# Optimization experiments

Measured on AMD Instinct MI355X. Metric: run time of the kernel, lower is better.

The kernel has to match this reference:

```python
import jax, jax.numpy as jnp
import numpy as np


def setup_inputs() -> dict:
    key = jax.random.key(0)
    kq, kk, kv = jax.random.split(key, 3)
    B, N, D = 8, 4096, 128
    Q = jax.random.normal(kq, (B, N, D), dtype=jnp.float32)
    K = jax.random.normal(kk, (B, N, D), dtype=jnp.float32)
    V = jax.random.normal(kv, (B, N, D), dtype=jnp.float32)
    return {"Q": Q, "K": K, "V": V}


def reference(Q, K, V):
    # attention = Q @ K^T  -> [B, N, N]  (scale=None, mask=None path)
    attention = jnp.einsum('bnd,bmd->bnm', Q, K)
    attention = jax.nn.softmax(attention, axis=-1)
    # context = attention @ V -> [B, N, D]
    context = jnp.einsum('bnm,bmd->bnd', attention, V)
    return context
```

## Files before the change

### kernel.cpp

```cpp
#include <hip/hip_runtime.h>

#define NB 8
#define SEQ 4096
#define DIM 128
#define BQ 128
#define KVB 64
#define NTILES (SEQ / KVB)
#define ROUNDS (NTILES / 2)
#define IMG_BYTES 32768
#define WS_NEED ((size_t)NB * NTILES * IMG_BYTES)
#define L2E 1.44269504088896f

typedef _Float16 f16x8 __attribute__((ext_vector_type(8)));
typedef __bf16 bf16x8 __attribute__((ext_vector_type(8)));
typedef float f32x4 __attribute__((ext_vector_type(4)));
typedef float f32x16 __attribute__((ext_vector_type(16)));

struct U4 { unsigned x, y, z, w; };

static __device__ __forceinline__ unsigned cvtpk_bf16(float a, float b) {
  unsigned d;
  asm("v_cvt_pk_bf16_f32 %0, %1, %2" : "=v"(d) : "v"(a), "v"(b));
  return d;
}

#define EXP2(x) __builtin_amdgcn_exp2f(x)

__global__ void prep_kv(const float* __restrict__ K, const float* __restrict__ V,
                        unsigned char* __restrict__ ws) {
  const int t = blockIdx.x;
  const int b = blockIdx.y;
  unsigned char* img = ws + ((size_t)b * NTILES + t) * IMG_BYTES;
  int4* kimg = (int4*)img;
  int4* vimg = (int4*)(img + 16384);
  const float* Kb = K + ((size_t)b * SEQ + t * KVB) * DIM;
  const float* Vb = V + ((size_t)b * SEQ + t * KVB) * DIM;
  const int tid = threadIdx.x;

#pragma unroll
  for (int p = 0; p < 4; ++p) {
    const int un = tid + 256 * p;
    const int kv = un >> 4;
    const int u = (un & 15) ^ (kv & 7);
    const int s = u >> 1, hh = u & 1;
    const float* src = Kb + (size_t)kv * DIM + 16 * s + 8 * hh;
    f16x8 hv;
#pragma unroll
    for (int j = 0; j < 8; ++j) hv[j] = (_Float16)src[j];
    kimg[un] = __builtin_bit_cast(int4, hv);
  }

#pragma unroll
  for (int p = 0; p < 4; ++p) {
    const int un = tid + 256 * p;
    const int d = un >> 3;
    const int u = (un & 7) ^ (d & 7);
    const int s2 = u >> 1, hh = u & 1;
    bf16x8 hv;
#pragma unroll
    for (int e = 0; e < 8; ++e) {
      const int kv = 16 * s2 + 4 * hh + (e & 3) + 8 * (e >> 2);
      hv[e] = (__bf16)Vb[(size_t)kv * DIM + d];
    }
    vimg[un] = __builtin_bit_cast(int4, hv);
  }
}

__global__ __launch_bounds__(512, 2)
void attn_fwd9(const float* __restrict__ Q, const unsigned char* __restrict__ ws,
               float* __restrict__ O) {
  __shared__ __align__(16) unsigned char smem[131072];

  const int tid = threadIdx.x;
  const int grp = tid >> 8;
  const int w4 = (tid >> 6) & 3;
  const int l = tid & 63;
  const int l31 = l & 31;
  const int h = l >> 5;

  const int bid = blockIdx.x;
  const int b = bid & 7;
  const int qt = bid >> 3;
  const size_t base = (size_t)b * SEQ * DIM;
  const int qrow = qt * BQ + w4 * 32 + l31;

  f16x8 qf[8];
  {
    const float* qp = Q + base + (size_t)qrow * DIM + 8 * h;
#pragma unroll
    for (int s = 0; s < 8; ++s) {
      f32x4 a = *(const f32x4*)(qp + 16 * s);
      f32x4 c = *(const f32x4*)(qp + 16 * s + 4);
      f16x8 hv;
#pragma unroll
      for (int j = 0; j < 4; ++j) {
        hv[j] = (_Float16)(a[j] * L2E);
        hv[j + 4] = (_Float16)(c[j] * L2E);
      }
      qf[s] = hv;
    }
  }

  f32x16 o[4];
#pragma unroll
  for (int j = 0; j < 4; ++j) {
#pragma unroll
    for (int r = 0; r < 16; ++r) o[j][r] = 0.f;
  }
  float ls = 0.f;

  unsigned char* mybuf = smem + grp * 65536;
  const unsigned char* wsb = ws + (size_t)b * NTILES * IMG_BYTES;

  auto STAGE = [&](int t, int bufsel) {
    const unsigned char* src = wsb + (size_t)t * IMG_BYTES + w4 * 8192 + l * 16;
    unsigned char* dst = mybuf + bufsel * 32768 + w4 * 8192;
#pragma unroll
    for (int i = 0; i < 8; ++i) {
      __builtin_amdgcn_global_load_lds(
          (const __attribute__((address_space(1))) unsigned int*)(src + i * 1024),
          (__attribute__((address_space(3))) unsigned int*)(dst + i * 1024),
          16, 0, 0);
    }
  };

  const int kb2 = (l31 * 256 + ((l & 7) * 16)) ^ (h * 16);
  const int vb2 = (16384 + l31 * 128 + ((l & 7) * 16)) ^ (h * 16);

  STAGE(grp, 0);
  __syncthreads();

  for (int i = 0; i < ROUNDS; ++i) {
    const int cur = i & 1;
    if (i + 1 < ROUNDS) STAGE(2 * (i + 1) + grp, cur ^ 1);
    const unsigned char* bufp = mybuf + cur * 32768;

    f32x16 s0, s1;
#pragma unroll
    for (int r = 0; r < 16; ++r) { s0[r] = 0.f; s1[r] = 0.f; }
    __builtin_amdgcn_s_setprio(1);
#pragma unroll
    for (int s = 0; s < 8; ++s) {
      const unsigned char* ka = bufp + (kb2 ^ (32 * s));
      f16x8 k0 = *(const f16x8*)(ka);
      f16x8 k1 = *(const f16x8*)(ka + 8192);
      s0 = __builtin_amdgcn_mfma_f32_32x32x16_f16(k0, qf[s], s0, 0, 0, 0);
      s1 = __builtin_amdgcn_mfma_f32_32x32x16_f16(k1, qf[s], s1, 0, 0, 0);
    }
    __builtin_amdgcn_s_setprio(0);

    float a0 = 0.f, a1 = 0.f, a2 = 0.f, a3 = 0.f;
#pragma unroll
    for (int r = 0; r < 16; r += 4) {
      s0[r + 0] = EXP2(s0[r + 0]);
      s0[r + 1] = EXP2(s0[r + 1]);
      s0[r + 2] = EXP2(s0[r + 2]);
      s0[r + 3] = EXP2(s0[r + 3]);
      a0 += s0[r + 0]; a1 += s0[r + 1]; a2 += s0[r + 2]; a3 += s0[r + 3];
    }
#pragma unroll
    for (int r = 0; r < 16; r += 4) {
      s1[r + 0] = EXP2(s1[r + 0]);
      s1[r + 1] = EXP2(s1[r + 1]);
      s1[r + 2] = EXP2(s1[r + 2]);
      s1[r + 3] = EXP2(s1[r + 3]);
      a0 += s1[r + 0]; a1 += s1[r + 1]; a2 += s1[r + 2]; a3 += s1[r + 3];
    }
    ls += (a0 + a1) + (a2 + a3);

    bf16x8 pb[2][2];
#pragma unroll
    for (int u = 0; u < 2; ++u) {
      U4 t0 = {cvtpk_bf16(s0[8 * u + 0], s0[8 * u + 1]),
               cvtpk_bf16(s0[8 * u + 2], s0[8 * u + 3]),
               cvtpk_bf16(s0[8 * u + 4], s0[8 * u + 5]),
               cvtpk_bf16(s0[8 * u + 6], s0[8 * u + 7])};
      U4 t1 = {cvtpk_bf16(s1[8 * u + 0], s1[8 * u + 1]),
               cvtpk_bf16(s1[8 * u + 2], s1[8 * u + 3]),
               cvtpk_bf16(s1[8 * u + 4], s1[8 * u + 5]),
               cvtpk_bf16(s1[8 * u + 6], s1[8 * u + 7])};
      pb[0][u] = __builtin_bit_cast(bf16x8, t0);
      pb[1][u] = __builtin_bit_cast(bf16x8, t1);
    }

    __builtin_amdgcn_s_setprio(1);
#pragma unroll
    for (int s2 = 0; s2 < 4; ++s2) {
      const unsigned char* va = bufp + (vb2 ^ (32 * s2));
      const bf16x8 pbb = pb[s2 >> 1][s2 & 1];
#pragma unroll
      for (int j = 0; j < 4; ++j) {
        bf16x8 vf = *(const bf16x8*)(va + j * 4096);
        o[j] = __builtin_amdgcn_mfma_f32_32x32x16_bf16(vf, pbb, o[j], 0, 0, 0);
      }
    }
    __builtin_amdgcn_s_setprio(0);
    __syncthreads();
  }

  ls += __shfl_xor(ls, 32);

  if (grp == 1) {
    int4* park = (int4*)(smem + w4 * 16384);
#pragma unroll
    for (int j = 0; j < 4; ++j) {
#pragma unroll
      for (int rq = 0; rq < 4; ++rq) {
        f32x4 part = {o[j][4 * rq + 0], o[j][4 * rq + 1], o[j][4 * rq + 2],
                      o[j][4 * rq + 3]};
        park[l * 16 + ((4 * j + rq) ^ (l & 7))] = __builtin_bit_cast(int4, part);
      }
    }
    if (h == 0) *(float*)(smem + 65536 + w4 * 128 + l31 * 4) = ls;
  }
  __syncthreads();

  if (grp == 0) {
    const float lsB = *(const float*)(smem + 65536 + w4 * 128 + l31 * 4);
    const float inv = 1.0f / (ls + lsB);
    const int4* park = (const int4*)(smem + w4 * 16384);
    float* Ob = O + base + (size_t)qrow * DIM;
#pragma unroll
    for (int j = 0; j < 4; ++j) {
#pragma unroll
      for (int rq = 0; rq < 4; ++rq) {
        const f32x4 ob =
            __builtin_bit_cast(f32x4, park[l * 16 + ((4 * j + rq) ^ (l & 7))]);
        f32x4 res;
#pragma unroll
        for (int r = 0; r < 4; ++r)
          res[r] = (o[j][4 * rq + r] + ob[r]) * inv;
        *(f32x4*)(Ob + 32 * j + 8 * rq + 4 * h) = res;
      }
    }
  }
}

extern "C" void kernel_launch(void* const* d_in, const int* in_sizes, int n_in,
                              void* d_out, int out_size, void* d_ws,
                              size_t ws_size, hipStream_t stream) {
  const float* Q = (const float*)d_in[0];
  const float* K = (const float*)d_in[1];
  const float* V = (const float*)d_in[2];
  float* Out = (float*)d_out;
  if (ws_size < WS_NEED) return;
  prep_kv<<<dim3(NTILES, NB), dim3(256), 0, stream>>>(K, V, (unsigned char*)d_ws);
  attn_fwd9<<<dim3(SEQ / BQ * NB), dim3(512), 0, stream>>>(
      Q, (const unsigned char*)d_ws, Out);
}
```

Measured before the change: 96.12 us.

## Widen K/V LDS swizzle to 16 and interleave softmax with PV MFMAs per sub-tile

Changes the K and V workspace image layout to use a 16-way XOR swizzle, with V laid out as 256-byte rows covering two 64-dim halves, to cut LDS bank conflicts on the fragment reads. It also splits the QK MFMA loop into two sequential chains and processes the first 32-key sub-tile's exp/convert/PV MFMAs before the second sub-tile's exp. The intent is to overlap transcendental work with matrix-core work and shorten dependency stalls. The risks are a longer serial MFMA chain in the QK step and higher register pressure from the precomputed V offsets.

New measurement: 94.47 us. No clear change (-1.7%).

```diff
diff --git a/kernel.cpp b/kernel.cpp
--- a/kernel.cpp
+++ b/kernel.cpp
@@ -41,7 +41,7 @@
   for (int p = 0; p < 4; ++p) {
     const int un = tid + 256 * p;
     const int kv = un >> 4;
-    const int u = (un & 15) ^ (kv & 7);
+    const int u = (un & 15) ^ (kv & 15);
     const int s = u >> 1, hh = u & 1;
     const float* src = Kb + (size_t)kv * DIM + 16 * s + 8 * hh;
     f16x8 hv;
@@ -53,9 +53,11 @@
 #pragma unroll
   for (int p = 0; p < 4; ++p) {
     const int un = tid + 256 * p;
-    const int d = un >> 3;
-    const int u = (un & 7) ^ (d & 7);
-    const int s2 = u >> 1, hh = u & 1;
+    const int rr = un >> 4;
+    const int c = (un & 15) ^ (rr & 15);
+    const int dhi = c >> 3, slot = c & 7;
+    const int s2 = slot >> 1, hh = slot & 1;
+    const int d = 64 * dhi + rr;
     bf16x8 hv;
 #pragma unroll
     for (int e = 0; e < 8; ++e) {
@@ -67,8 +69,8 @@
 }
 
 __global__ __launch_bounds__(512, 2)
-void attn_fwd9(const float* __restrict__ Q, const unsigned char* __restrict__ ws,
-               float* __restrict__ O) {
+void attn_fwd10(const float* __restrict__ Q, const unsigned char* __restrict__ ws,
+                float* __restrict__ O) {
   __shared__ __align__(16) unsigned char smem[131072];
 
   const int tid = threadIdx.x;
@@ -124,8 +126,13 @@
     }
   };
 
-  const int kb2 = (l31 * 256 + ((l & 7) * 16)) ^ (h * 16);
-  const int vb2 = (16384 + l31 * 128 + ((l & 7) * 16)) ^ (h * 16);
+  const int kb2 = (l31 * 256 + ((l31 & 15) * 16)) ^ (h * 16);
+  int vb[4];
+#pragma unroll
+  for (int j = 0; j < 4; ++j) {
+    const int rr = 32 * (j & 1) + l31;
+    vb[j] = 16384 + rr * 256 + ((((j >> 1) * 8 + h) ^ (rr & 15)) * 16);
+  }
 
   STAGE(grp, 0);
   __syncthreads();
@@ -141,10 +148,12 @@
     __builtin_amdgcn_s_setprio(1);
 #pragma unroll
     for (int s = 0; s < 8; ++s) {
-      const unsigned char* ka = bufp + (kb2 ^ (32 * s));
-      f16x8 k0 = *(const f16x8*)(ka);
-      f16x8 k1 = *(const f16x8*)(ka + 8192);
+      f16x8 k0 = *(const f16x8*)(bufp + (kb2 ^ (32 * s)));
       s0 = __builtin_amdgcn_mfma_f32_32x32x16_f16(k0, qf[s], s0, 0, 0, 0);
+    }
+#pragma unroll
+    for (int s = 0; s < 8; ++s) {
+      f16x8 k1 = *(const f16x8*)(bufp + (kb2 ^ (32 * s)) + 8192);
       s1 = __builtin_amdgcn_mfma_f32_32x32x16_f16(k1, qf[s], s1, 0, 0, 0);
     }
     __builtin_amdgcn_s_setprio(0);
@@ -158,6 +167,27 @@
       s0[r + 3] = EXP2(s0[r + 3]);
       a0 += s0[r + 0]; a1 += s0[r + 1]; a2 += s0[r + 2]; a3 += s0[r + 3];
     }
+    bf16x8 pb0[2];
+#pragma unroll
+    for (int u = 0; u < 2; ++u) {
+      U4 t0 = {cvtpk_bf16(s0[8 * u + 0], s0[8 * u + 1]),
+               cvtpk_bf16(s0[8 * u + 2], s0[8 * u + 3]),
+               cvtpk_bf16(s0[8 * u + 4], s0[8 * u + 5]),
+               cvtpk_bf16(s0[8 * u + 6], s0[8 * u + 7])};
+      pb0[u] = __builtin_bit_cast(bf16x8, t0);
+    }
+
+    __builtin_amdgcn_s_setprio(1);
+#pragma unroll
+    for (int s2 = 0; s2 < 2; ++s2) {
+#pragma unroll
+      for (int j = 0; j < 4; ++j) {
+        bf16x8 vf = *(const bf16x8*)(bufp + (vb[j] ^ (32 * s2)));
+        o[j] = __builtin_amdgcn_mfma_f32_32x32x16_bf16(vf, pb0[s2], o[j], 0, 0, 0);
+      }
+    }
+    __builtin_amdgcn_s_setprio(0);
+
 #pragma unroll
     for (int r = 0; r < 16; r += 4) {
       s1[r + 0] = EXP2(s1[r + 0]);
@@ -167,31 +197,23 @@
       a0 += s1[r + 0]; a1 += s1[r + 1]; a2 += s1[r + 2]; a3 += s1[r + 3];
     }
     ls += (a0 + a1) + (a2 + a3);
-
-    bf16x8 pb[2][2];
+    bf16x8 pb1[2];
 #pragma unroll
     for (int u = 0; u < 2; ++u) {
-      U4 t0 = {cvtpk_bf16(s0[8 * u + 0], s0[8 * u + 1]),
-               cvtpk_bf16(s0[8 * u + 2], s0[8 * u + 3]),
-               cvtpk_bf16(s0[8 * u + 4], s0[8 * u + 5]),
-               cvtpk_bf16(s0[8 * u + 6], s0[8 * u + 7])};
       U4 t1 = {cvtpk_bf16(s1[8 * u + 0], s1[8 * u + 1]),
                cvtpk_bf16(s1[8 * u + 2], s1[8 * u + 3]),
                cvtpk_bf16(s1[8 * u + 4], s1[8 * u + 5]),
                cvtpk_bf16(s1[8 * u + 6], s1[8 * u + 7])};
-      pb[0][u] = __builtin_bit_cast(bf16x8, t0);
-      pb[1][u] = __builtin_bit_cast(bf16x8, t1);
+      pb1[u] = __builtin_bit_cast(bf16x8, t1);
     }
 
     __builtin_amdgcn_s_setprio(1);
 #pragma unroll
-    for (int s2 = 0; s2 < 4; ++s2) {
-      const unsigned char* va = bufp + (vb2 ^ (32 * s2));
-      const bf16x8 pbb = pb[s2 >> 1][s2 & 1];
+    for (int s2 = 2; s2 < 4; ++s2) {
 #pragma unroll
       for (int j = 0; j < 4; ++j) {
-        bf16x8 vf = *(const bf16x8*)(va + j * 4096);
-        o[j] = __builtin_amdgcn_mfma_f32_32x32x16_bf16(vf, pbb, o[j], 0, 0, 0);
+        bf16x8 vf = *(const bf16x8*)(bufp + (vb[j] ^ (32 * s2)));
+        o[j] = __builtin_amdgcn_mfma_f32_32x32x16_bf16(vf, pb1[s2 - 2], o[j], 0, 0, 0);
       }
     }
     __builtin_amdgcn_s_setprio(0);
@@ -245,6 +267,6 @@
   float* Out = (float*)d_out;
   if (ws_size < WS_NEED) return;
   prep_kv<<<dim3(NTILES, NB), dim3(256), 0, stream>>>(K, V, (unsigned char*)d_ws);
-  attn_fwd9<<<dim3(SEQ / BQ * NB), dim3(512), 0, stream>>>(
+  attn_fwd10<<<dim3(SEQ / BQ * NB), dim3(512), 0, stream>>>(
       Q, (const unsigned char*)d_ws, Out);
 }
```

## Split KV loop across four wave groups with 32-row tiles and staged reduction

Applied to the files above, without the earlier changes.

Each block now has 1024 threads in four wave groups. Each group processes interleaved 32-row KV tiles instead of two groups on 64-row tiles, and the prep kernel's K/V image layout and swizzle are reworked to match. Per-wave accumulators are combined through a serialized four-stage LDS reduction before normalization and the store. The goal is more waves in flight per query tile to hide latency. In exchange there are more barriers, a longer epilogue reduction, and fewer blocks resident per CU (launch_bounds drops the min-2-blocks hint while LDS use stays at 128KB).

Measured after the change: 117.1 us. 21.9% more time.

```diff
diff --git a/kernel.cpp b/kernel.cpp
--- a/kernel.cpp
+++ b/kernel.cpp
@@ -4,10 +4,10 @@
 #define SEQ 4096
 #define DIM 128
 #define BQ 128
-#define KVB 64
+#define KVB 32
 #define NTILES (SEQ / KVB)
-#define ROUNDS (NTILES / 2)
-#define IMG_BYTES 32768
+#define ROUNDS (NTILES / 4)
+#define IMG_BYTES 16384
 #define WS_NEED ((size_t)NB * NTILES * IMG_BYTES)
 #define L2E 1.44269504088896f
 
@@ -32,17 +32,17 @@
   const int b = blockIdx.y;
   unsigned char* img = ws + ((size_t)b * NTILES + t) * IMG_BYTES;
   int4* kimg = (int4*)img;
-  int4* vimg = (int4*)(img + 16384);
+  int4* vimg = (int4*)(img + 8192);
   const float* Kb = K + ((size_t)b * SEQ + t * KVB) * DIM;
   const float* Vb = V + ((size_t)b * SEQ + t * KVB) * DIM;
   const int tid = threadIdx.x;
 
 #pragma unroll
-  for (int p = 0; p < 4; ++p) {
+  for (int p = 0; p < 2; ++p) {
     const int un = tid + 256 * p;
     const int kv = un >> 4;
-    const int u = (un & 15) ^ (kv & 7);
-    const int s = u >> 1, hh = u & 1;
+    const int c = (un & 15) ^ (kv & 15);
+    const int s = c >> 1, hh = c & 1;
     const float* src = Kb + (size_t)kv * DIM + 16 * s + 8 * hh;
     f16x8 hv;
 #pragma unroll
@@ -51,11 +51,12 @@
   }
 
 #pragma unroll
-  for (int p = 0; p < 4; ++p) {
+  for (int p = 0; p < 2; ++p) {
     const int un = tid + 256 * p;
-    const int d = un >> 3;
-    const int u = (un & 7) ^ (d & 7);
-    const int s2 = u >> 1, hh = u & 1;
+    const int rr = un >> 4;
+    const int c = (un & 15) ^ (rr & 15);
+    const int dhi = c >> 2, s2 = (c >> 1) & 1, hh = c & 1;
+    const int d = 32 * dhi + rr;
     bf16x8 hv;
 #pragma unroll
     for (int e = 0; e < 8; ++e) {
@@ -66,14 +67,15 @@
   }
 }
 
-__global__ __launch_bounds__(512, 2)
-void attn_fwd9(const float* __restrict__ Q, const unsigned char* __restrict__ ws,
-               float* __restrict__ O) {
+__global__ __launch_bounds__(1024)
+void attn_fwd11(const float* __restrict__ Q, const unsigned char* __restrict__ ws,
+                float* __restrict__ O) {
   __shared__ __align__(16) unsigned char smem[131072];
 
   const int tid = threadIdx.x;
-  const int grp = tid >> 8;
-  const int w4 = (tid >> 6) & 3;
+  const int w = tid >> 6;
+  const int g = w >> 2;
+  const int wg = w & 3;
   const int l = tid & 63;
   const int l31 = l & 31;
   const int h = l >> 5;
@@ -82,7 +84,7 @@
   const int b = bid & 7;
   const int qt = bid >> 3;
   const size_t base = (size_t)b * SEQ * DIM;
-  const int qrow = qt * BQ + w4 * 32 + l31;
+  const int qrow = qt * BQ + wg * 32 + l31;
 
   f16x8 qf[8];
   {
@@ -109,89 +111,71 @@
   }
   float ls = 0.f;
 
-  unsigned char* mybuf = smem + grp * 65536;
+  unsigned char* mybuf = smem + g * 32768;
   const unsigned char* wsb = ws + (size_t)b * NTILES * IMG_BYTES;
 
   auto STAGE = [&](int t, int bufsel) {
-    const unsigned char* src = wsb + (size_t)t * IMG_BYTES + w4 * 8192 + l * 16;
-    unsigned char* dst = mybuf + bufsel * 32768 + w4 * 8192;
-#pragma unroll
-    for (int i = 0; i < 8; ++i) {
+    const unsigned char* src = wsb + (size_t)t * IMG_BYTES + wg * 4096 + l * 16;
+    unsigned char* dst = mybuf + bufsel * 16384 + wg * 4096;
+#pragma unroll
+    for (int i2 = 0; i2 < 4; ++i2) {
       __builtin_amdgcn_global_load_lds(
-          (const __attribute__((address_space(1))) unsigned int*)(src + i * 1024),
-          (__attribute__((address_space(3))) unsigned int*)(dst + i * 1024),
+          (const __attribute__((address_space(1))) unsigned int*)(src + i2 * 1024),
+          (__attribute__((address_space(3))) unsigned int*)(dst + i2 * 1024),
           16, 0, 0);
     }
   };
 
-  const int kb2 = (l31 * 256 + ((l & 7) * 16)) ^ (h * 16);
-  const int vb2 = (16384 + l31 * 128 + ((l & 7) * 16)) ^ (h * 16);
-
-  STAGE(grp, 0);
+  const int lbase = l31 * 256 + ((((l31 & 15)) << 4) ^ (h << 4));
+
+  STAGE(g, 0);
   __syncthreads();
 
   for (int i = 0; i < ROUNDS; ++i) {
     const int cur = i & 1;
-    if (i + 1 < ROUNDS) STAGE(2 * (i + 1) + grp, cur ^ 1);
-    const unsigned char* bufp = mybuf + cur * 32768;
-
-    f32x16 s0, s1;
-#pragma unroll
-    for (int r = 0; r < 16; ++r) { s0[r] = 0.f; s1[r] = 0.f; }
+    if (i + 1 < ROUNDS) STAGE(4 * (i + 1) + g, cur ^ 1);
+    const unsigned char* bufp = mybuf + cur * 16384;
+
+    f32x16 s;
+#pragma unroll
+    for (int r = 0; r < 16; ++r) s[r] = 0.f;
     __builtin_amdgcn_s_setprio(1);
 #pragma unroll
-    for (int s = 0; s < 8; ++s) {
-      const unsigned char* ka = bufp + (kb2 ^ (32 * s));
-      f16x8 k0 = *(const f16x8*)(ka);
-      f16x8 k1 = *(const f16x8*)(ka + 8192);
-      s0 = __builtin_amdgcn_mfma_f32_32x32x16_f16(k0, qf[s], s0, 0, 0, 0);
-      s1 = __builtin_amdgcn_mfma_f32_32x32x16_f16(k1, qf[s], s1, 0, 0, 0);
+    for (int s8 = 0; s8 < 8; ++s8) {
+      f16x8 kf = *(const f16x8*)(bufp + (lbase ^ (s8 << 5)));
+      s = __builtin_amdgcn_mfma_f32_32x32x16_f16(kf, qf[s8], s, 0, 0, 0);
     }
     __builtin_amdgcn_s_setprio(0);
 
     float a0 = 0.f, a1 = 0.f, a2 = 0.f, a3 = 0.f;
 #pragma unroll
     for (int r = 0; r < 16; r += 4) {
-      s0[r + 0] = EXP2(s0[r + 0]);
-      s0[r + 1] = EXP2(s0[r + 1]);
-      s0[r + 2] = EXP2(s0[r + 2]);
-      s0[r + 3] = EXP2(s0[r + 3]);
-      a0 += s0[r + 0]; a1 += s0[r + 1]; a2 += s0[r + 2]; a3 += s0[r + 3];
-    }
-#pragma unroll
-    for (int r = 0; r < 16; r += 4) {
-      s1[r + 0] = EXP2(s1[r + 0]);
-      s1[r + 1] = EXP2(s1[r + 1]);
-      s1[r + 2] = EXP2(s1[r + 2]);
-      s1[r + 3] = EXP2(s1[r + 3]);
-      a0 += s1[r + 0]; a1 += s1[r + 1]; a2 += s1[r + 2]; a3 += s1[r + 3];
+      s[r + 0] = EXP2(s[r + 0]);
+      s[r + 1] = EXP2(s[r + 1]);
+      s[r + 2] = EXP2(s[r + 2]);
+      s[r + 3] = EXP2(s[r + 3]);
+      a0 += s[r + 0]; a1 += s[r + 1]; a2 += s[r + 2]; a3 += s[r + 3];
     }
     ls += (a0 + a1) + (a2 + a3);
 
-    bf16x8 pb[2][2];
+    bf16x8 pb[2];
 #pragma unroll
     for (int u = 0; u < 2; ++u) {
-      U4 t0 = {cvtpk_bf16(s0[8 * u + 0], s0[8 * u + 1]),
-               cvtpk_bf16(s0[8 * u + 2], s0[8 * u + 3]),
-               cvtpk_bf16(s0[8 * u + 4], s0[8 * u + 5]),
-               cvtpk_bf16(s0[8 * u + 6], s0[8 * u + 7])};
-      U4 t1 = {cvtpk_bf16(s1[8 * u + 0], s1[8 * u + 1]),
-               cvtpk_bf16(s1[8 * u + 2], s1[8 * u + 3]),
-               cvtpk_bf16(s1[8 * u + 4], s1[8 * u + 5]),
-               cvtpk_bf16(s1[8 * u + 6], s1[8 * u + 7])};
-      pb[0][u] = __builtin_bit_cast(bf16x8, t0);
-      pb[1][u] = __builtin_bit_cast(bf16x8, t1);
+      U4 t0 = {cvtpk_bf16(s[8 * u + 0], s[8 * u + 1]),
+               cvtpk_bf16(s[8 * u + 2], s[8 * u + 3]),
+               cvtpk_bf16(s[8 * u + 4], s[8 * u + 5]),
+               cvtpk_bf16(s[8 * u + 6], s[8 * u + 7])};
+      pb[u] = __builtin_bit_cast(bf16x8, t0);
     }
 
     __builtin_amdgcn_s_setprio(1);
 #pragma unroll
-    for (int s2 = 0; s2 < 4; ++s2) {
-      const unsigned char* va = bufp + (vb2 ^ (32 * s2));
-      const bf16x8 pbb = pb[s2 >> 1][s2 & 1];
+    for (int s2 = 0; s2 < 2; ++s2) {
 #pragma unroll
       for (int j = 0; j < 4; ++j) {
-        bf16x8 vf = *(const bf16x8*)(va + j * 4096);
-        o[j] = __builtin_amdgcn_mfma_f32_32x32x16_bf16(vf, pbb, o[j], 0, 0, 0);
+        bf16x8 vf = *(const bf16x8*)(bufp + 8192 +
+                                     (lbase ^ (j << 6) ^ (s2 << 5)));
+        o[j] = __builtin_amdgcn_mfma_f32_32x32x16_bf16(vf, pb[s2], o[j], 0, 0, 0);
       }
     }
     __builtin_amdgcn_s_setprio(0);
@@ -200,39 +184,58 @@
 
   ls += __shfl_xor(ls, 32);
 
-  if (grp == 1) {
-    int4* park = (int4*)(smem + w4 * 16384);
-#pragma unroll
-    for (int j = 0; j < 4; ++j) {
-#pragma unroll
-      for (int rq = 0; rq < 4; ++rq) {
-        f32x4 part = {o[j][4 * rq + 0], o[j][4 * rq + 1], o[j][4 * rq + 2],
-                      o[j][4 * rq + 3]};
-        park[l * 16 + ((4 * j + rq) ^ (l & 7))] = __builtin_bit_cast(int4, part);
+  int4* park = (int4*)(smem + wg * 16384);
+  float* lsp = (float*)(smem + 65536);
+  const int lsi = wg * 32 + l31;
+
+  __syncthreads();
+#pragma unroll 1
+  for (int stage = 0; stage < 4; ++stage) {
+    if (g == stage) {
+      if (stage == 0) {
+#pragma unroll
+        for (int j = 0; j < 4; ++j) {
+#pragma unroll
+          for (int rq = 0; rq < 4; ++rq) {
+            f32x4 part = {o[j][4 * rq + 0], o[j][4 * rq + 1],
+                          o[j][4 * rq + 2], o[j][4 * rq + 3]};
+            park[l * 16 + ((4 * j + rq) ^ (l & 7))] =
+                __builtin_bit_cast(int4, part);
+          }
+        }
+        if (h == 0) lsp[lsi] = ls;
+      } else if (stage < 3) {
+#pragma unroll
+        for (int j = 0; j < 4; ++j) {
+#pragma unroll
+          for (int rq = 0; rq < 4; ++rq) {
+            const int idx = l * 16 + ((4 * j + rq) ^ (l & 7));
+            f32x4 acc = __builtin_bit_cast(f32x4, park[idx]);
+#pragma unroll
+            for (int r = 0; r < 4; ++r) acc[r] += o[j][4 * rq + r];
+            park[idx] = __builtin_bit_cast(int4, acc);
+          }
+        }
+        if (h == 0) lsp[lsi] += ls;
+      } else {
+        const float inv = 1.0f / (lsp[lsi] + ls);
+        float* Ob = O + base + (size_t)qrow * DIM;
+#pragma unroll
+        for (int j = 0; j < 4; ++j) {
+#pragma unroll
+          for (int rq = 0; rq < 4; ++rq) {
+            const f32x4 acc = __builtin_bit_cast(
+                f32x4, park[l * 16 + ((4 * j + rq) ^ (l & 7))]);
+            f32x4 res;
+#pragma unroll
+            for (int r = 0; r < 4; ++r)
+              res[r] = (acc[r] + o[j][4 * rq + r]) * inv;
+            *(f32x4*)(Ob + 32 * j + 8 * rq + 4 * h) = res;
+          }
+        }
       }
     }
-    if (h == 0) *(float*)(smem + 65536 + w4 * 128 + l31 * 4) = ls;
-  }
-  __syncthreads();
-
-  if (grp == 0) {
-    const float lsB = *(const float*)(smem + 65536 + w4 * 128 + l31 * 4);
-    const float inv = 1.0f / (ls + lsB);
-    const int4* park = (const int4*)(smem + w4 * 16384);
-    float* Ob = O + base + (size_t)qrow * DIM;
-#pragma unroll
-    for (int j = 0; j < 4; ++j) {
-#pragma unroll
-      for (int rq = 0; rq < 4; ++rq) {
-        const f32x4 ob =
-            __builtin_bit_cast(f32x4, park[l * 16 + ((4 * j + rq) ^ (l & 7))]);
-        f32x4 res;
-#pragma unroll
-        for (int r = 0; r < 4; ++r)
-          res[r] = (o[j][4 * rq + r] + ob[r]) * inv;
-        *(f32x4*)(Ob + 32 * j + 8 * rq + 4 * h) = res;
-      }
-    }
+    __syncthreads();
   }
 }
 
@@ -245,6 +248,6 @@
   float* Out = (float*)d_out;
   if (ws_size < WS_NEED) return;
   prep_kv<<<dim3(NTILES, NB), dim3(256), 0, stream>>>(K, V, (unsigned char*)d_ws);
-  attn_fwd9<<<dim3(SEQ / BQ * NB), dim3(512), 0, stream>>>(
+  attn_fwd11<<<dim3(SEQ / BQ * NB), dim3(1024), 0, stream>>>(
       Q, (const unsigned char*)d_ws, Out);
 }
```
